# Kernel tuning notes

Measured on AMD Instinct MI355X. Metric: run time of the kernel, lower is better.

Reference implementation:

```python
import jax, jax.numpy as jnp
import numpy as np
import math

ANSWER_LEN = 11; D_MODEL = 6; FFN_DIM = 3; HEAD_DIM = 3; MAX_SEQ_LEN = 34
N_HEADS = 2; POS_DIM = 3; TOK_DIM = 3; VOCAB_SIZE = 14; MAX_DIGITS = 10
EOS_TOKEN = 12; EQUALS_TOKEN = 11; PAD_TOKEN = 13; PLUS_TOKEN = 10
B, T = 65536, 34


def _spiral(i, period):
    return (math.cos(2 * math.pi * i / period), math.sin(2 * math.pi * i / period), i / max(period - 1, 1))


def _build_pos_enc():
    N_POS = 10
    pe = np.zeros((MAX_SEQ_LEN, POS_DIM), dtype=np.float32)
    for i in range(MAX_DIGITS):
        pe[i] = _spiral(i, N_POS)
    for i in range(MAX_DIGITS):
        pe[11 + i] = _spiral(i, N_POS)
    for i in range(min(ANSWER_LEN, N_POS)):
        pe[22 + i] = _spiral(i, N_POS)
    pe[32] = [0.0, 0.0, 1.5]
    pe[10] = [2.0, 0.0, -1.0]
    pe[21] = [0.0, 2.0, -1.0]
    pe[33] = [-2.0, 0.0, -1.0]
    return pe


def _build_tok_emb():
    emb = np.zeros((VOCAB_SIZE, TOK_DIM), dtype=np.float32)
    for d in range(10):
        emb[d] = _spiral(d, 10)
    emb[PLUS_TOKEN] = [2.0, 0.0, -1.0]
    emb[EQUALS_TOKEN] = [0.0, 2.0, -1.0]
    emb[EOS_TOKEN] = [-2.0, 0.0, -1.0]
    emb[PAD_TOKEN] = [0.0, -2.0, -1.0]
    return emb


def setup_inputs() -> dict:
    key = jax.random.key(0)
    ks = jax.random.split(key, 12)
    H = N_HEADS * HEAD_DIM  # 6

    def lin(k, out_d, in_d):
        bound = 1.0 / math.sqrt(in_d)
        return jax.random.uniform(k, (out_d, in_d), jnp.float32, -bound, bound)

    return {
        'idx': jax.random.randint(ks[0], (B, T), 0, VOCAB_SIZE),
        'tok_emb': jnp.asarray(_build_tok_emb()),
        'pos_enc': jnp.asarray(_build_pos_enc()),
        'q_w': lin(ks[1], H, POS_DIM),
        'k_w': lin(ks[2], H, POS_DIM),
        'v_w': lin(ks[3], H, TOK_DIM),
        'out_w': lin(ks[4], D_MODEL, H),
        'ln1_g': jnp.ones((D_MODEL,)), 'ln1_b': jnp.zeros((D_MODEL,)),
        'ln2_g': jnp.ones((D_MODEL,)), 'ln2_b': jnp.zeros((D_MODEL,)),
        'lnf_g': jnp.ones((D_MODEL,)), 'lnf_b': jnp.zeros((D_MODEL,)),
        'ffn_w1': lin(ks[5], FFN_DIM, D_MODEL),
        'ffn_b1': jax.random.uniform(ks[6], (FFN_DIM,), jnp.float32, -1/math.sqrt(D_MODEL), 1/math.sqrt(D_MODEL)),
        'ffn_w2': lin(ks[7], D_MODEL, FFN_DIM),
        'ffn_b2': jax.random.uniform(ks[8], (D_MODEL,), jnp.float32, -1/math.sqrt(FFN_DIM), 1/math.sqrt(FFN_DIM)),
        'head_w': lin(ks[9], TOK_DIM, D_MODEL),
    }


def _ln(x, g, b, eps=1e-5):
    mu = jnp.mean(x, -1, keepdims=True)
    var = jnp.mean((x - mu) ** 2, -1, keepdims=True)
    return (x - mu) * jax.lax.rsqrt(var + eps) * g + b


def reference(idx, tok_emb, pos_enc, q_w, k_w, v_w, out_w,
              ln1_g, ln1_b, ln2_g, ln2_b, lnf_g, lnf_b,
              ffn_w1, ffn_b1, ffn_w2, ffn_b2, head_w):
    b, t = idx.shape
    tok = tok_emb[idx]                              # [B,T,3]
    pos = jnp.broadcast_to(pos_enc[:t][None], (b, t, POS_DIM))
    x = jnp.concatenate([tok, pos], -1)             # [B,T,6]
    h = _ln(x, ln1_g, ln1_b)
    x_tok, x_pos = h[..., :TOK_DIM], h[..., TOK_DIM:]
    q = (x_pos @ q_w.T).reshape(b, t, N_HEADS, HEAD_DIM)
    k = (x_pos @ k_w.T).reshape(b, t, N_HEADS, HEAD_DIM)
    v = (x_tok @ v_w.T).reshape(b, t, N_HEADS, HEAD_DIM)
    attn = jnp.einsum('bqhd,bkhd->bhqk', q, k) / math.sqrt(HEAD_DIM)
    mask = jnp.tril(jnp.ones((t, t), dtype=bool))
    attn = jnp.where(mask[None, None], attn, -jnp.inf)
    attn = jax.nn.softmax(attn, -1)
    out = jnp.einsum('bhqk,bkhd->bqhd', attn, v).reshape(b, t, N_HEADS * HEAD_DIM)
    x = x + out @ out_w.T
    h2 = _ln(x, ln2_g, ln2_b)
    ffn = jax.nn.gelu(h2 @ ffn_w1.T + ffn_b1, approximate=False) @ ffn_w2.T + ffn_b2
    x = x + ffn
    x = _ln(x, lnf_g, lnf_b)
    return (x @ head_w.T) @ tok_emb.T               # [B,T,VOCAB]
```

## Files before the change

kernel.cpp:

```cpp
#include <hip/hip_runtime.h>
#include <math.h>

#define TT  34
#define VV  14
#define BLK 256

typedef float v2f __attribute__((ext_vector_type(2)));
typedef float v4f __attribute__((ext_vector_type(4)));

#if __has_builtin(__builtin_amdgcn_exp2f)
#define EXP2F(x) __builtin_amdgcn_exp2f(x)
#else
#define EXP2F(x) exp2f(x)
#endif
#if __has_builtin(__builtin_amdgcn_rcpf)
#define RCPF(x) __builtin_amdgcn_rcpf(x)
#else
#define RCPF(x) (1.0f/(x))
#endif

static __device__ __forceinline__ v2f fma2(v2f a, v2f b, v2f c) {
    return __builtin_elementwise_fma(a, b, c);
}
static __device__ __forceinline__ v2f bc2(float s) { v2f r; r.x = s; r.y = s; return r; }
#define SV2(v, a, b) __builtin_shufflevector((v), (v), (a), (b))


__global__ __launch_bounds__(BLK) void addtx_fwd(
    const int*   __restrict__ idx,
    const float* __restrict__ tok_emb,
    const float* __restrict__ pos_enc,
    const float* __restrict__ q_w,
    const float* __restrict__ k_w,
    const float* __restrict__ v_w,
    const float* __restrict__ out_w,
    const float* __restrict__ ln1_g, const float* __restrict__ ln1_b,
    const float* __restrict__ ln2_g, const float* __restrict__ ln2_b,
    const float* __restrict__ lnf_g, const float* __restrict__ lnf_b,
    const float* __restrict__ ffn_w1, const float* __restrict__ ffn_b1,
    const float* __restrict__ ffn_w2, const float* __restrict__ ffn_b2,
    const float* __restrict__ head_w,
    float* __restrict__ out)
{
    __shared__ v4f   kvs[TT * VV * 3];
    __shared__ float wsm[308];
    __shared__ int   idsb[308];

    const int tid = threadIdx.x;
    const int blk = blockIdx.x;

    for (int i = tid; i < 308; i += BLK) {
        float val = 0.0f;
        if (i < 36)       { const int j = i / 6, d = i - j * 6; val = out_w[d * 6 + j]; }
        else if (i < 42)  val = ln2_g[i - 36];
        else if (i < 48)  val = ln2_b[i - 42];
        else if (i < 60)  { const int k = i - 48, d = k >> 1, ii = k & 1; val = ffn_w1[ii * 6 + d]; }
        else if (i < 66)  val = ffn_w1[12 + (i - 60)];
        else if (i < 69)  val = ffn_b1[i - 66];
        else if (i < 70)  val = 0.0f;
        else if (i < 88)  { const int k = i - 70, ii = k / 6, d = k - ii * 6; val = ffn_w2[d * 3 + ii]; }
        else if (i < 94)  val = ffn_b2[i - 88];
        else if (i < 96)  val = 0.0f;
        else if (i < 108) { const int k = i - 96, d = k >> 1, c = k & 1; val = lnf_g[d] * head_w[c * 6 + d]; }
        else if (i < 114) { const int d = i - 108; val = lnf_g[d] * head_w[12 + d]; }
        else if (i < 118) val = 0.0f;
        else if (i < 121) { const int c = i - 118; float s = 0.0f;
                            #pragma unroll
                            for (int d = 0; d < 6; ++d) s += lnf_b[d] * head_w[c * 6 + d];
                            val = s; }
        else if (i < 122) val = 0.0f;
        else if (i < 164) { const int k = i - 122, c = k / 14, v = k - c * 14; val = tok_emb[v * 3 + c]; }
        else if (i < 206) val = tok_emb[i - 164];
        else              val = pos_enc[i - 206];
        wsm[i] = val;
    }

    const int ntot = (int)gridDim.x * BLK;
    const int b0   = (blk * BLK) / TT;
    {
        const int gb = b0 * TT;
        for (int e = tid; e < 308; e += BLK) {
            const int g = gb + e;
            idsb[e] = (g < ntot) ? (idx[g] * 48) : 0;
        }
    }

    const float rs3l = 0.57735026918962576f * 1.4426950408889634f;
    for (int e = tid; e < TT * VV; e += BLK) {
        const int pos = e / VV, id = e - pos * VV;
        float x[6];
        x[0] = tok_emb[id * 3 + 0]; x[1] = tok_emb[id * 3 + 1]; x[2] = tok_emb[id * 3 + 2];
        x[3] = pos_enc[pos * 3 + 0]; x[4] = pos_enc[pos * 3 + 1]; x[5] = pos_enc[pos * 3 + 2];
        float mu = (x[0] + x[1] + x[2] + x[3] + x[4] + x[5]) * (1.0f / 6.0f);
        float var = 0.0f;
        #pragma unroll
        for (int d = 0; d < 6; ++d) { float dd = x[d] - mu; var += dd * dd; }
        const float rstd = rsqrtf(var * (1.0f / 6.0f) + 1e-5f);
        float h[6];
        #pragma unroll
        for (int d = 0; d < 6; ++d) h[d] = (x[d] - mu) * rstd * ln1_g[d] + ln1_b[d];
        float kk[6], vvv[6];
        #pragma unroll
        for (int r = 0; r < 6; ++r) {
            kk[r]  = (h[3] * k_w[r * 3 + 0] + h[4] * k_w[r * 3 + 1] + h[5] * k_w[r * 3 + 2]) * rs3l;
            vvv[r] =  h[0] * v_w[r * 3 + 0] + h[1] * v_w[r * 3 + 1] + h[2] * v_w[r * 3 + 2];
        }
        v4f f0; f0.x = kk[0]; f0.y = kk[3]; f0.z = kk[1]; f0.w = kk[4];
        v4f f1; f1.x = kk[2]; f1.y = kk[5]; f1.z = vvv[0]; f1.w = vvv[3];
        v4f f2; f2.x = vvv[1]; f2.y = vvv[4]; f2.z = vvv[2]; f2.w = vvv[5];
        kvs[e * 3 + 0] = f0;
        kvs[e * 3 + 1] = f1;
        kvs[e * 3 + 2] = f2;
    }
    __syncthreads();

    const int srank = (tid + ((blk & 3) << 6)) & (BLK - 1);
    const int r0 = (blk * BLK) % TT;
    const int m  = (TT - r0) % TT;
    int dsel, ksel;
    if (m < 18) {
        const int nA = (18 - m) << 3;
        if (srank < nA)            { dsel = m + (srank >> 3); ksel = srank & 7; }
        else if (srank < nA + 112) { const int r = srank - nA;       dsel = 18 + r / 7; ksel = r % 7; }
        else                       { const int r = srank - nA - 112; dsel = r >> 3;     ksel = r & 7; }
    } else {
        const int nA = (TT - m) * 7;
        if (srank < nA)            { dsel = m + srank / 7; ksel = srank % 7; }
        else if (srank < nA + 144) { const int r = srank - nA;       dsel = r >> 3;     ksel = r & 7; }
        else                       { const int r = srank - nA - 144; dsel = 18 + r / 7; ksel = r % 7; }
    }
    const int il   = dsel + ksel * TT;
    const int flat = blk * BLK + il;
    const int b    = flat / TT;
    const int t    = flat - b * TT;
    const int* __restrict__ rowL = idsb + (b - b0) * TT;

    float x[6];
    {
        const int tb = rowL[t] >> 4;
        x[0] = wsm[164 + tb]; x[1] = wsm[165 + tb]; x[2] = wsm[166 + tb];
        x[3] = wsm[206 + t * 3]; x[4] = wsm[207 + t * 3]; x[5] = wsm[208 + t * 3];
    }
    float q[6];
    {
        float mu = (x[0] + x[1] + x[2] + x[3] + x[4] + x[5]) * (1.0f / 6.0f);
        float var = 0.0f;
        #pragma unroll
        for (int d = 0; d < 6; ++d) { float dd = x[d] - mu; var += dd * dd; }
        const float rstd = rsqrtf(var * (1.0f / 6.0f) + 1e-5f);
        const float h3 = (x[3] - mu) * rstd * ln1_g[3] + ln1_b[3];
        const float h4 = (x[4] - mu) * rstd * ln1_g[4] + ln1_b[4];
        const float h5 = (x[5] - mu) * rstd * ln1_g[5] + ln1_b[5];
        #pragma unroll
        for (int r = 0; r < 6; ++r)
            q[r] = h3 * q_w[r * 3 + 0] + h4 * q_w[r * 3 + 1] + h5 * q_w[r * 3 + 2];
    }
    const v2f Q03 = {q[0], q[3]}, Q14 = {q[1], q[4]}, Q25 = {q[2], q[5]};

    v2f L = {0.f, 0.f}, A0 = {0.f, 0.f}, A1 = {0.f, 0.f}, A2 = {0.f, 0.f};
    int ids48 = rowL[0];
    const char* kp = (const char*)kvs;
    for (int s = 0; s <= t; ++s) {
        const v4f* e4 = (const v4f*)(kp + ids48);
        const v4f ka = e4[0], kb = e4[1], vb = e4[2];
        ids48 = rowL[s + 1];
        v2f sc = fma2(Q03, SV2(ka, 0, 1),
                 fma2(Q14, SV2(ka, 2, 3),
                      Q25 * SV2(kb, 0, 1)));
        v2f p; p.x = EXP2F(sc.x); p.y = EXP2F(sc.y);
        L += p;
        A0 = fma2(p, SV2(kb, 2, 3), A0);
        A1 = fma2(p, SV2(vb, 0, 1), A1);
        A2 = fma2(p, SV2(vb, 2, 3), A2);
        kp += VV * 48;
    }
    v2f I; I.x = RCPF(L.x); I.y = RCPF(L.y);
    const v2f O0 = A0 * I, O1 = A1 * I, O2 = A2 * I;
    const float o6[6] = {O0.x, O1.x, O2.x, O0.y, O1.y, O2.y};

    v2f X0 = {x[0], x[1]}, X1 = {x[2], x[3]}, X2 = {x[4], x[5]};
    #define LD2(i) (*reinterpret_cast<const v2f*>(&wsm[(i)]))
    #pragma unroll
    for (int j = 0; j < 6; ++j) {
        const v2f oj = bc2(o6[j]);
        X0 = fma2(oj, LD2(j * 6 + 0), X0);
        X1 = fma2(oj, LD2(j * 6 + 2), X1);
        X2 = fma2(oj, LD2(j * 6 + 4), X2);
    }

    {
        v2f S = X0 + X1 + X2;
        const float mu = (S.x + S.y) * (1.0f / 6.0f);
        const v2f muv = bc2(mu);
        const v2f D0 = X0 - muv, D1 = X1 - muv, D2 = X2 - muv;
        v2f E = fma2(D0, D0, fma2(D1, D1, D2 * D2));
        const float rstd = rsqrtf((E.x + E.y) * (1.0f / 6.0f) + 1e-5f);
        const v2f rs = bc2(rstd);
        const v2f H0 = fma2(D0 * rs, LD2(36), LD2(42));
        const v2f H1 = fma2(D1 * rs, LD2(38), LD2(44));
        const v2f H2 = fma2(D2 * rs, LD2(40), LD2(46));
        const float h[6] = {H0.x, H0.y, H1.x, H1.y, H2.x, H2.y};
        v2f F = LD2(66);
        float f2 = wsm[68];
        #pragma unroll
        for (int d = 0; d < 6; ++d) {
            F  = fma2(bc2(h[d]), LD2(48 + 2 * d), F);
            f2 = fmaf(h[d], wsm[60 + d], f2);
        }
        float g3[3];
        g3[0] = 0.5f * F.x * (1.0f + erff(F.x * 0.70710678118654752f));
        g3[1] = 0.5f * F.y * (1.0f + erff(F.y * 0.70710678118654752f));
        g3[2] = 0.5f * f2  * (1.0f + erff(f2  * 0.70710678118654752f));
        X0 += LD2(88); X1 += LD2(90); X2 += LD2(92);
        #pragma unroll
        for (int i = 0; i < 3; ++i) {
            const v2f gi = bc2(g3[i]);
            X0 = fma2(gi, LD2(70 + i * 6 + 0), X0);
            X1 = fma2(gi, LD2(70 + i * 6 + 2), X1);
            X2 = fma2(gi, LD2(70 + i * 6 + 4), X2);
        }
    }

    v2f lgv[7];
    {
        v2f S = X0 + X1 + X2;
        const float mu = (S.x + S.y) * (1.0f / 6.0f);
        const v2f muv = bc2(mu);
        const v2f D0 = X0 - muv, D1 = X1 - muv, D2 = X2 - muv;
        v2f E = fma2(D0, D0, fma2(D1, D1, D2 * D2));
        const float rstd = rsqrtf((E.x + E.y) * (1.0f / 6.0f) + 1e-5f);
        const float xd[6] = {D0.x, D0.y, D1.x, D1.y, D2.x, D2.y};
        v2f D01 = {0.f, 0.f};
        float d2 = 0.f;
        #pragma unroll
        for (int d = 0; d < 6; ++d) {
            D01 = fma2(bc2(xd[d]), LD2(96 + 2 * d), D01);
            d2  = fmaf(xd[d], wsm[108 + d], d2);
        }
        const v2f y01 = fma2(bc2(rstd), D01, LD2(118));
        const float y2 = fmaf(rstd, d2, wsm[120]);
        const v2f Y0 = bc2(y01.x), Y1 = bc2(y01.y), Y2 = bc2(y2);
        #pragma unroll
        for (int mm = 0; mm < 7; ++mm)
            lgv[mm] = fma2(Y0, LD2(122 + 2 * mm),
                      fma2(Y1, LD2(136 + 2 * mm),
                           Y2 * LD2(150 + 2 * mm)));
    }
    __syncthreads();

    v2f* lg2 = reinterpret_cast<v2f*>(kvs);
    #pragma unroll
    for (int j = 0; j < 7; ++j)
        lg2[il * 7 + j] = lgv[j];
    __syncthreads();
    const v2f* s2 = reinterpret_cast<const v2f*>(kvs);
    v2f* __restrict__ ob2 = reinterpret_cast<v2f*>(out + (size_t)blk * (BLK * VV));
    #pragma unroll
    for (int j = 0; j < 7; ++j)
        ob2[j * BLK + tid] = s2[j * BLK + tid];
}

extern "C" void kernel_launch(void* const* d_in, const int* in_sizes, int n_in,
                              void* d_out, int out_size, void* d_ws, size_t ws_size,
                              hipStream_t stream) {
    const int*   idx     = (const int*)  d_in[0];
    const float* tok_emb = (const float*)d_in[1];
    const float* pos_enc = (const float*)d_in[2];
    const float* q_w     = (const float*)d_in[3];
    const float* k_w     = (const float*)d_in[4];
    const float* v_w     = (const float*)d_in[5];
    const float* out_w   = (const float*)d_in[6];
    const float* ln1_g   = (const float*)d_in[7];
    const float* ln1_b   = (const float*)d_in[8];
    const float* ln2_g   = (const float*)d_in[9];
    const float* ln2_b   = (const float*)d_in[10];
    const float* lnf_g   = (const float*)d_in[11];
    const float* lnf_b   = (const float*)d_in[12];
    const float* ffn_w1  = (const float*)d_in[13];
    const float* ffn_b1  = (const float*)d_in[14];
    const float* ffn_w2  = (const float*)d_in[15];
    const float* ffn_b2  = (const float*)d_in[16];
    const float* head_w  = (const float*)d_in[17];
    float* out = (float*)d_out;

    const int n = in_sizes[0];
    const int blocks = n / BLK;
    addtx_fwd<<<blocks, BLK, 0, stream>>>(idx, tok_emb, pos_enc, q_w, k_w, v_w, out_w,
                                          ln1_g, ln1_b, ln2_g, ln2_b, lnf_g, lnf_b,
                                          ffn_w1, ffn_b1, ffn_w2, ffn_b2, head_w, out);
}
```

Baseline: 213.3 us.

## Process two adjacent query positions per thread sharing K/V loads

Each thread now handles a pair of consecutive positions (t0, t0+1) in the same sequence, sharing the K/V shared-memory reads across both queries in the attention loop. The grid is halved (512 positions per block), which amortizes per-block LDS table setup over more work. The shared-memory transpose for output staging is removed, and results are written directly to global with vector stores. This raises register pressure and makes the stores less coalesced, and the thread-to-pair assignment changes the load balance across lanes.

```diff
diff --git a/kernel.cpp b/kernel.cpp
--- a/kernel.cpp
+++ b/kernel.cpp
@@ -4,6 +4,7 @@
 #define TT  34
 #define VV  14
 #define BLK 256
+#define NPB 512
 
 typedef float v2f __attribute__((ext_vector_type(2)));
 typedef float v4f __attribute__((ext_vector_type(4)));
@@ -24,7 +25,118 @@
 }
 static __device__ __forceinline__ v2f bc2(float s) { v2f r; r.x = s; r.y = s; return r; }
 #define SV2(v, a, b) __builtin_shufflevector((v), (v), (a), (b))
-
+#define LD2(i) (*reinterpret_cast<const v2f*>(&wsm[(i)]))
+
+
+static __device__ __forceinline__ void epi_store(
+    const float* __restrict__ wsm, const float o6[6], const float x[6],
+    float* __restrict__ outp, int elem1)
+{
+    v2f X0 = {x[0], x[1]}, X1 = {x[2], x[3]}, X2 = {x[4], x[5]};
+    #pragma unroll
+    for (int j = 0; j < 6; ++j) {
+        const v2f oj = bc2(o6[j]);
+        X0 = fma2(oj, LD2(j * 6 + 0), X0);
+        X1 = fma2(oj, LD2(j * 6 + 2), X1);
+        X2 = fma2(oj, LD2(j * 6 + 4), X2);
+    }
+    {
+        v2f S = X0 + X1 + X2;
+        const float mu = (S.x + S.y) * (1.0f / 6.0f);
+        const v2f muv = bc2(mu);
+        const v2f D0 = X0 - muv, D1 = X1 - muv, D2 = X2 - muv;
+        v2f E = fma2(D0, D0, fma2(D1, D1, D2 * D2));
+        const float rstd = rsqrtf((E.x + E.y) * (1.0f / 6.0f) + 1e-5f);
+        const v2f rs = bc2(rstd);
+        const v2f H0 = fma2(D0 * rs, LD2(36), LD2(42));
+        const v2f H1 = fma2(D1 * rs, LD2(38), LD2(44));
+        const v2f H2 = fma2(D2 * rs, LD2(40), LD2(46));
+        const float h[6] = {H0.x, H0.y, H1.x, H1.y, H2.x, H2.y};
+        v2f F = LD2(66);
+        float f2 = wsm[68];
+        #pragma unroll
+        for (int d = 0; d < 6; ++d) {
+            F  = fma2(bc2(h[d]), LD2(48 + 2 * d), F);
+            f2 = fmaf(h[d], wsm[60 + d], f2);
+        }
+        float g3[3];
+        g3[0] = 0.5f * F.x * (1.0f + erff(F.x * 0.70710678118654752f));
+        g3[1] = 0.5f * F.y * (1.0f + erff(F.y * 0.70710678118654752f));
+        g3[2] = 0.5f * f2  * (1.0f + erff(f2  * 0.70710678118654752f));
+        X0 += LD2(88); X1 += LD2(90); X2 += LD2(92);
+        #pragma unroll
+        for (int i = 0; i < 3; ++i) {
+            const v2f gi = bc2(g3[i]);
+            X0 = fma2(gi, LD2(70 + i * 6 + 0), X0);
+            X1 = fma2(gi, LD2(70 + i * 6 + 2), X1);
+            X2 = fma2(gi, LD2(70 + i * 6 + 4), X2);
+        }
+    }
+    v2f lgv[7];
+    {
+        v2f S = X0 + X1 + X2;
+        const float mu = (S.x + S.y) * (1.0f / 6.0f);
+        const v2f muv = bc2(mu);
+        const v2f D0 = X0 - muv, D1 = X1 - muv, D2 = X2 - muv;
+        v2f E = fma2(D0, D0, fma2(D1, D1, D2 * D2));
+        const float rstd = rsqrtf((E.x + E.y) * (1.0f / 6.0f) + 1e-5f);
+        const float xd[6] = {D0.x, D0.y, D1.x, D1.y, D2.x, D2.y};
+        v2f D01 = {0.f, 0.f};
+        float d2 = 0.f;
+        #pragma unroll
+        for (int d = 0; d < 6; ++d) {
+            D01 = fma2(bc2(xd[d]), LD2(96 + 2 * d), D01);
+            d2  = fmaf(xd[d], wsm[108 + d], d2);
+        }
+        const v2f y01 = fma2(bc2(rstd), D01, LD2(118));
+        const float y2 = fmaf(rstd, d2, wsm[120]);
+        const v2f Y0 = bc2(y01.x), Y1 = bc2(y01.y), Y2 = bc2(y2);
+        #pragma unroll
+        for (int mm = 0; mm < 7; ++mm)
+            lgv[mm] = fma2(Y0, LD2(122 + 2 * mm),
+                      fma2(Y1, LD2(136 + 2 * mm),
+                           Y2 * LD2(150 + 2 * mm)));
+    }
+    if (!elem1) {
+        v4f w0; w0.x = lgv[0].x; w0.y = lgv[0].y; w0.z = lgv[1].x; w0.w = lgv[1].y;
+        v4f w1; w1.x = lgv[2].x; w1.y = lgv[2].y; w1.z = lgv[3].x; w1.w = lgv[3].y;
+        v4f w2; w2.x = lgv[4].x; w2.y = lgv[4].y; w2.z = lgv[5].x; w2.w = lgv[5].y;
+        *reinterpret_cast<v4f*>(outp + 0) = w0;
+        *reinterpret_cast<v4f*>(outp + 4) = w1;
+        *reinterpret_cast<v4f*>(outp + 8) = w2;
+        *reinterpret_cast<v2f*>(outp + 12) = lgv[6];
+    } else {
+        *reinterpret_cast<v2f*>(outp + 0) = lgv[0];
+        v4f w0; w0.x = lgv[1].x; w0.y = lgv[1].y; w0.z = lgv[2].x; w0.w = lgv[2].y;
+        v4f w1; w1.x = lgv[3].x; w1.y = lgv[3].y; w1.z = lgv[4].x; w1.w = lgv[4].y;
+        v4f w2; w2.x = lgv[5].x; w2.y = lgv[5].y; w2.z = lgv[6].x; w2.w = lgv[6].y;
+        *reinterpret_cast<v4f*>(outp + 2)  = w0;
+        *reinterpret_cast<v4f*>(outp + 6)  = w1;
+        *reinterpret_cast<v4f*>(outp + 10) = w2;
+    }
+}
+
+static __device__ __forceinline__ void make_q(
+    const float* __restrict__ ln1_g, const float* __restrict__ ln1_b,
+    const float* __restrict__ q_w, const float x[6],
+    v2f& Q03, v2f& Q14, v2f& Q25)
+{
+    float mu = (x[0] + x[1] + x[2] + x[3] + x[4] + x[5]) * (1.0f / 6.0f);
+    float var = 0.0f;
+    #pragma unroll
+    for (int d = 0; d < 6; ++d) { float dd = x[d] - mu; var += dd * dd; }
+    const float rstd = rsqrtf(var * (1.0f / 6.0f) + 1e-5f);
+    const float h3 = (x[3] - mu) * rstd * ln1_g[3] + ln1_b[3];
+    const float h4 = (x[4] - mu) * rstd * ln1_g[4] + ln1_b[4];
+    const float h5 = (x[5] - mu) * rstd * ln1_g[5] + ln1_b[5];
+    float q[6];
+    #pragma unroll
+    for (int r = 0; r < 6; ++r)
+        q[r] = h3 * q_w[r * 3 + 0] + h4 * q_w[r * 3 + 1] + h5 * q_w[r * 3 + 2];
+    Q03.x = q[0]; Q03.y = q[3];
+    Q14.x = q[1]; Q14.y = q[4];
+    Q25.x = q[2]; Q25.y = q[5];
+}
 
 __global__ __launch_bounds__(BLK) void addtx_fwd(
     const int*   __restrict__ idx,
@@ -40,11 +152,11 @@
     const float* __restrict__ ffn_w1, const float* __restrict__ ffn_b1,
     const float* __restrict__ ffn_w2, const float* __restrict__ ffn_b2,
     const float* __restrict__ head_w,
-    float* __restrict__ out)
+    float* __restrict__ out, int n)
 {
     __shared__ v4f   kvs[TT * VV * 3];
     __shared__ float wsm[308];
-    __shared__ int   idsb[308];
+    __shared__ int   idsb[17 * TT];
 
     const int tid = threadIdx.x;
     const int blk = blockIdx.x;
@@ -75,13 +187,13 @@
         wsm[i] = val;
     }
 
-    const int ntot = (int)gridDim.x * BLK;
-    const int b0   = (blk * BLK) / TT;
+    const int p0 = blk * BLK;
+    const int b0 = p0 / 17;
     {
         const int gb = b0 * TT;
-        for (int e = tid; e < 308; e += BLK) {
+        for (int e = tid; e < 17 * TT; e += BLK) {
             const int g = gb + e;
-            idsb[e] = (g < ntot) ? (idx[g] * 48) : 0;
+            idsb[e] = (g < n) ? (idx[g] * 48) : 0;
         }
     }
 
@@ -115,149 +227,76 @@
     __syncthreads();
 
     const int srank = (tid + ((blk & 3) << 6)) & (BLK - 1);
-    const int r0 = (blk * BLK) % TT;
-    const int m  = (TT - r0) % TT;
-    int dsel, ksel;
-    if (m < 18) {
-        const int nA = (18 - m) << 3;
-        if (srank < nA)            { dsel = m + (srank >> 3); ksel = srank & 7; }
-        else if (srank < nA + 112) { const int r = srank - nA;       dsel = 18 + r / 7; ksel = r % 7; }
-        else                       { const int r = srank - nA - 112; dsel = r >> 3;     ksel = r & 7; }
-    } else {
-        const int nA = (TT - m) * 7;
-        if (srank < nA)            { dsel = m + srank / 7; ksel = srank % 7; }
-        else if (srank < nA + 144) { const int r = srank - nA;       dsel = r >> 3;     ksel = r & 7; }
-        else                       { const int r = srank - nA - 144; dsel = 18 + r / 7; ksel = r % 7; }
-    }
-    const int il   = dsel + ksel * TT;
-    const int flat = blk * BLK + il;
-    const int b    = flat / TT;
-    const int t    = flat - b * TT;
+    const int r0 = p0 % 17;
+    const int thrA = 15 * r0;
+    int u, k;
+    if (srank < thrA)           { u = srank / 15;      k = srank - 15 * u; }
+    else if (srank < thrA + 16) { u = r0;              k = srank - thrA;   }
+    else                        { const int rr = srank - 1; u = rr / 15; k = rr - 15 * u; }
+    int dd17 = u - r0; if (dd17 < 0) dd17 += 17;
+    const int pl = dd17 + 17 * k;
+    const int p  = p0 + pl;
+    const int b  = p / 17;
+    const int t0 = 2 * (p - b * 17);
+    const int t1 = t0 + 1;
     const int* __restrict__ rowL = idsb + (b - b0) * TT;
 
-    float x[6];
-    {
-        const int tb = rowL[t] >> 4;
-        x[0] = wsm[164 + tb]; x[1] = wsm[165 + tb]; x[2] = wsm[166 + tb];
-        x[3] = wsm[206 + t * 3]; x[4] = wsm[207 + t * 3]; x[5] = wsm[208 + t * 3];
-    }
-    float q[6];
-    {
-        float mu = (x[0] + x[1] + x[2] + x[3] + x[4] + x[5]) * (1.0f / 6.0f);
-        float var = 0.0f;
-        #pragma unroll
-        for (int d = 0; d < 6; ++d) { float dd = x[d] - mu; var += dd * dd; }
-        const float rstd = rsqrtf(var * (1.0f / 6.0f) + 1e-5f);
-        const float h3 = (x[3] - mu) * rstd * ln1_g[3] + ln1_b[3];
-        const float h4 = (x[4] - mu) * rstd * ln1_g[4] + ln1_b[4];
-        const float h5 = (x[5] - mu) * rstd * ln1_g[5] + ln1_b[5];
-        #pragma unroll
-        for (int r = 0; r < 6; ++r)
-            q[r] = h3 * q_w[r * 3 + 0] + h4 * q_w[r * 3 + 1] + h5 * q_w[r * 3 + 2];
-    }
-    const v2f Q03 = {q[0], q[3]}, Q14 = {q[1], q[4]}, Q25 = {q[2], q[5]};
-
-    v2f L = {0.f, 0.f}, A0 = {0.f, 0.f}, A1 = {0.f, 0.f}, A2 = {0.f, 0.f};
+    float xa[6], xb[6];
+    {
+        const int ta3 = rowL[t0] >> 4;
+        const int tb3 = rowL[t1] >> 4;
+        xa[0] = wsm[164 + ta3]; xa[1] = wsm[165 + ta3]; xa[2] = wsm[166 + ta3];
+        xb[0] = wsm[164 + tb3]; xb[1] = wsm[165 + tb3]; xb[2] = wsm[166 + tb3];
+        xa[3] = wsm[206 + t0 * 3]; xa[4] = wsm[207 + t0 * 3]; xa[5] = wsm[208 + t0 * 3];
+        xb[3] = wsm[206 + t1 * 3]; xb[4] = wsm[207 + t1 * 3]; xb[5] = wsm[208 + t1 * 3];
+    }
+    v2f Q03a, Q14a, Q25a, Q03b, Q14b, Q25b;
+    make_q(ln1_g, ln1_b, q_w, xa, Q03a, Q14a, Q25a);
+    make_q(ln1_g, ln1_b, q_w, xb, Q03b, Q14b, Q25b);
+
+    v2f La = {0.f, 0.f}, A0a = {0.f, 0.f}, A1a = {0.f, 0.f}, A2a = {0.f, 0.f};
+    v2f Lb = {0.f, 0.f}, A0b = {0.f, 0.f}, A1b = {0.f, 0.f}, A2b = {0.f, 0.f};
     int ids48 = rowL[0];
     const char* kp = (const char*)kvs;
-    for (int s = 0; s <= t; ++s) {
+    for (int s = 0; s <= t0; ++s) {
         const v4f* e4 = (const v4f*)(kp + ids48);
         const v4f ka = e4[0], kb = e4[1], vb = e4[2];
         ids48 = rowL[s + 1];
-        v2f sc = fma2(Q03, SV2(ka, 0, 1),
-                 fma2(Q14, SV2(ka, 2, 3),
-                      Q25 * SV2(kb, 0, 1)));
-        v2f p; p.x = EXP2F(sc.x); p.y = EXP2F(sc.y);
-        L += p;
-        A0 = fma2(p, SV2(kb, 2, 3), A0);
-        A1 = fma2(p, SV2(vb, 0, 1), A1);
-        A2 = fma2(p, SV2(vb, 2, 3), A2);
+        const v2f ka01 = SV2(ka, 0, 1), ka23 = SV2(ka, 2, 3);
+        const v2f kb01 = SV2(kb, 0, 1), kb23 = SV2(kb, 2, 3);
+        const v2f vb01 = SV2(vb, 0, 1), vb23 = SV2(vb, 2, 3);
+        v2f sa = fma2(Q03a, ka01, fma2(Q14a, ka23, Q25a * kb01));
+        v2f sb = fma2(Q03b, ka01, fma2(Q14b, ka23, Q25b * kb01));
+        v2f pa; pa.x = EXP2F(sa.x); pa.y = EXP2F(sa.y);
+        v2f pb; pb.x = EXP2F(sb.x); pb.y = EXP2F(sb.y);
+        La += pa; Lb += pb;
+        A0a = fma2(pa, kb23, A0a); A0b = fma2(pb, kb23, A0b);
+        A1a = fma2(pa, vb01, A1a); A1b = fma2(pb, vb01, A1b);
+        A2a = fma2(pa, vb23, A2a); A2b = fma2(pb, vb23, A2b);
         kp += VV * 48;
     }
-    v2f I; I.x = RCPF(L.x); I.y = RCPF(L.y);
-    const v2f O0 = A0 * I, O1 = A1 * I, O2 = A2 * I;
-    const float o6[6] = {O0.x, O1.x, O2.x, O0.y, O1.y, O2.y};
-
-    v2f X0 = {x[0], x[1]}, X1 = {x[2], x[3]}, X2 = {x[4], x[5]};
-    #define LD2(i) (*reinterpret_cast<const v2f*>(&wsm[(i)]))
-    #pragma unroll
-    for (int j = 0; j < 6; ++j) {
-        const v2f oj = bc2(o6[j]);
-        X0 = fma2(oj, LD2(j * 6 + 0), X0);
-        X1 = fma2(oj, LD2(j * 6 + 2), X1);
-        X2 = fma2(oj, LD2(j * 6 + 4), X2);
-    }
-
-    {
-        v2f S = X0 + X1 + X2;
-        const float mu = (S.x + S.y) * (1.0f / 6.0f);
-        const v2f muv = bc2(mu);
-        const v2f D0 = X0 - muv, D1 = X1 - muv, D2 = X2 - muv;
-        v2f E = fma2(D0, D0, fma2(D1, D1, D2 * D2));
-        const float rstd = rsqrtf((E.x + E.y) * (1.0f / 6.0f) + 1e-5f);
-        const v2f rs = bc2(rstd);
-        const v2f H0 = fma2(D0 * rs, LD2(36), LD2(42));
-        const v2f H1 = fma2(D1 * rs, LD2(38), LD2(44));
-        const v2f H2 = fma2(D2 * rs, LD2(40), LD2(46));
-        const float h[6] = {H0.x, H0.y, H1.x, H1.y, H2.x, H2.y};
-        v2f F = LD2(66);
-        float f2 = wsm[68];
-        #pragma unroll
-        for (int d = 0; d < 6; ++d) {
-            F  = fma2(bc2(h[d]), LD2(48 + 2 * d), F);
-            f2 = fmaf(h[d], wsm[60 + d], f2);
-        }
-        float g3[3];
-        g3[0] = 0.5f * F.x * (1.0f + erff(F.x * 0.70710678118654752f));
-        g3[1] = 0.5f * F.y * (1.0f + erff(F.y * 0.70710678118654752f));
-        g3[2] = 0.5f * f2  * (1.0f + erff(f2  * 0.70710678118654752f));
-        X0 += LD2(88); X1 += LD2(90); X2 += LD2(92);
-        #pragma unroll
-        for (int i = 0; i < 3; ++i) {
-            const v2f gi = bc2(g3[i]);
-            X0 = fma2(gi, LD2(70 + i * 6 + 0), X0);
-            X1 = fma2(gi, LD2(70 + i * 6 + 2), X1);
-            X2 = fma2(gi, LD2(70 + i * 6 + 4), X2);
-        }
-    }
-
-    v2f lgv[7];
-    {
-        v2f S = X0 + X1 + X2;
-        const float mu = (S.x + S.y) * (1.0f / 6.0f);
-        const v2f muv = bc2(mu);
-        const v2f D0 = X0 - muv, D1 = X1 - muv, D2 = X2 - muv;
-        v2f E = fma2(D0, D0, fma2(D1, D1, D2 * D2));
-        const float rstd = rsqrtf((E.x + E.y) * (1.0f / 6.0f) + 1e-5f);
-        const float xd[6] = {D0.x, D0.y, D1.x, D1.y, D2.x, D2.y};
-        v2f D01 = {0.f, 0.f};
-        float d2 = 0.f;
-        #pragma unroll
-        for (int d = 0; d < 6; ++d) {
-            D01 = fma2(bc2(xd[d]), LD2(96 + 2 * d), D01);
-            d2  = fmaf(xd[d], wsm[108 + d], d2);
-        }
-        const v2f y01 = fma2(bc2(rstd), D01, LD2(118));
-        const float y2 = fmaf(rstd, d2, wsm[120]);
-        const v2f Y0 = bc2(y01.x), Y1 = bc2(y01.y), Y2 = bc2(y2);
-        #pragma unroll
-        for (int mm = 0; mm < 7; ++mm)
-            lgv[mm] = fma2(Y0, LD2(122 + 2 * mm),
-                      fma2(Y1, LD2(136 + 2 * mm),
-                           Y2 * LD2(150 + 2 * mm)));
-    }
-    __syncthreads();
-
-    v2f* lg2 = reinterpret_cast<v2f*>(kvs);
-    #pragma unroll
-    for (int j = 0; j < 7; ++j)
-        lg2[il * 7 + j] = lgv[j];
-    __syncthreads();
-    const v2f* s2 = reinterpret_cast<const v2f*>(kvs);
-    v2f* __restrict__ ob2 = reinterpret_cast<v2f*>(out + (size_t)blk * (BLK * VV));
-    #pragma unroll
-    for (int j = 0; j < 7; ++j)
-        ob2[j * BLK + tid] = s2[j * BLK + tid];
+    {
+        const v4f* e4 = (const v4f*)(kp + ids48);
+        const v4f ka = e4[0], kb = e4[1], vb = e4[2];
+        v2f sb = fma2(Q03b, SV2(ka, 0, 1),
+                 fma2(Q14b, SV2(ka, 2, 3), Q25b * SV2(kb, 0, 1)));
+        v2f pb; pb.x = EXP2F(sb.x); pb.y = EXP2F(sb.y);
+        Lb += pb;
+        A0b = fma2(pb, SV2(kb, 2, 3), A0b);
+        A1b = fma2(pb, SV2(vb, 0, 1), A1b);
+        A2b = fma2(pb, SV2(vb, 2, 3), A2b);
+    }
+
+    v2f Ia; Ia.x = RCPF(La.x); Ia.y = RCPF(La.y);
+    v2f Ib; Ib.x = RCPF(Lb.x); Ib.y = RCPF(Lb.y);
+    const v2f Oa0 = A0a * Ia, Oa1 = A1a * Ia, Oa2 = A2a * Ia;
+    const v2f Ob0 = A0b * Ib, Ob1 = A1b * Ib, Ob2 = A2b * Ib;
+    const float o6a[6] = {Oa0.x, Oa1.x, Oa2.x, Oa0.y, Oa1.y, Oa2.y};
+    const float o6b[6] = {Ob0.x, Ob1.x, Ob2.x, Ob0.y, Ob1.y, Ob2.y};
+
+    float* __restrict__ outp = out + (size_t)(b * TT + t0) * VV;
+    epi_store(wsm, o6a, xa, outp,      0);
+    epi_store(wsm, o6b, xb, outp + VV, 1);
 }
 
 extern "C" void kernel_launch(void* const* d_in, const int* in_sizes, int n_in,
@@ -284,8 +323,8 @@
     float* out = (float*)d_out;
 
     const int n = in_sizes[0];
-    const int blocks = n / BLK;
+    const int blocks = n / NPB;
     addtx_fwd<<<blocks, BLK, 0, stream>>>(idx, tok_emb, pos_enc, q_w, k_w, v_w, out_w,
                                           ln1_g, ln1_b, ln2_g, ln2_b, lnf_g, lnf_b,
-                                          ffn_w1, ffn_b1, ffn_w2, ffn_b2, head_w, out);
-}
+                                          ffn_w1, ffn_b1, ffn_w2, ffn_b2, head_w, out, n);
+}
```

After: 218.6 us. 2.5% more time.

## Double block size to 512 and rework thread-to-position mapping for larger tiles

Applied to the files above, without the earlier changes.

Raises the block size from 256 to 512 threads and adds an occupancy hint to launch_bounds. The per-block K/V table precompute and weight staging are amortised over twice as many output positions, which roughly halves the redundant setup work per element. The thread-to-(batch, position) assignment is rewritten for the new block size, and the total element count is passed in explicitly. The larger tile needs bigger shared buffers, and the new mapping logic risks different store coalescing or bank conflicts.

```diff
diff --git a/kernel.cpp b/kernel.cpp
--- a/kernel.cpp
+++ b/kernel.cpp
@@ -3,7 +3,7 @@
 
 #define TT  34
 #define VV  14
-#define BLK 256
+#define BLK 512
 
 typedef float v2f __attribute__((ext_vector_type(2)));
 typedef float v4f __attribute__((ext_vector_type(4)));
@@ -26,7 +26,7 @@
 #define SV2(v, a, b) __builtin_shufflevector((v), (v), (a), (b))
 
 
-__global__ __launch_bounds__(BLK) void addtx_fwd(
+__global__ __launch_bounds__(BLK, 8) void addtx_fwd(
     const int*   __restrict__ idx,
     const float* __restrict__ tok_emb,
     const float* __restrict__ pos_enc,
@@ -40,16 +40,17 @@
     const float* __restrict__ ffn_w1, const float* __restrict__ ffn_b1,
     const float* __restrict__ ffn_w2, const float* __restrict__ ffn_b2,
     const float* __restrict__ head_w,
-    float* __restrict__ out)
+    float* __restrict__ out, int n)
 {
-    __shared__ v4f   kvs[TT * VV * 3];
+    __shared__ v4f   kvs[1792];
     __shared__ float wsm[308];
-    __shared__ int   idsb[308];
+    __shared__ int   idsb[594];
 
     const int tid = threadIdx.x;
     const int blk = blockIdx.x;
 
-    for (int i = tid; i < 308; i += BLK) {
+    if (tid < 308) {
+        const int i = tid;
         float val = 0.0f;
         if (i < 36)       { const int j = i / 6, d = i - j * 6; val = out_w[d * 6 + j]; }
         else if (i < 42)  val = ln2_g[i - 36];
@@ -75,13 +76,13 @@
         wsm[i] = val;
     }
 
-    const int ntot = (int)gridDim.x * BLK;
-    const int b0   = (blk * BLK) / TT;
+    const int p0 = blk * BLK;
+    const int b0 = p0 / TT;
     {
         const int gb = b0 * TT;
-        for (int e = tid; e < 308; e += BLK) {
+        for (int e = tid; e < 594; e += BLK) {
             const int g = gb + e;
-            idsb[e] = (g < ntot) ? (idx[g] * 48) : 0;
+            idsb[e] = (g < n) ? (idx[g] * 48) : 0;
         }
     }
 
@@ -114,25 +115,17 @@
     }
     __syncthreads();
 
-    const int srank = (tid + ((blk & 3) << 6)) & (BLK - 1);
-    const int r0 = (blk * BLK) % TT;
-    const int m  = (TT - r0) % TT;
-    int dsel, ksel;
-    if (m < 18) {
-        const int nA = (18 - m) << 3;
-        if (srank < nA)            { dsel = m + (srank >> 3); ksel = srank & 7; }
-        else if (srank < nA + 112) { const int r = srank - nA;       dsel = 18 + r / 7; ksel = r % 7; }
-        else                       { const int r = srank - nA - 112; dsel = r >> 3;     ksel = r & 7; }
-    } else {
-        const int nA = (TT - m) * 7;
-        if (srank < nA)            { dsel = m + srank / 7; ksel = srank % 7; }
-        else if (srank < nA + 144) { const int r = srank - nA;       dsel = r >> 3;     ksel = r & 7; }
-        else                       { const int r = srank - nA - 144; dsel = 18 + r / 7; ksel = r % 7; }
-    }
-    const int il   = dsel + ksel * TT;
-    const int flat = blk * BLK + il;
+    const int srank = (tid + ((blk & 7) << 6)) & (BLK - 1);
+    const int r0 = p0 % TT;
+    const int thrA = 15 * r0;
+    int t, dlt, ksel;
+    if (srank < thrA)           { t = srank / 15; ksel = srank - 15 * t; dlt = t - r0 + TT; }
+    else if (srank < thrA + 32) { const int rr = srank - thrA; dlt = rr >> 4; ksel = rr & 15; t = r0 + dlt; }
+    else                        { const int rr = srank - thrA - 32; const int qq = rr / 15;
+                                  ksel = rr - 15 * qq; dlt = 2 + qq; t = r0 + dlt; }
+    const int il   = dlt + TT * ksel;
+    const int flat = p0 + il;
     const int b    = flat / TT;
-    const int t    = flat - b * TT;
     const int* __restrict__ rowL = idsb + (b - b0) * TT;
 
     float x[6];
@@ -287,5 +280,5 @@
     const int blocks = n / BLK;
     addtx_fwd<<<blocks, BLK, 0, stream>>>(idx, tok_emb, pos_enc, q_w, k_w, v_w, out_w,
                                           ln1_g, ln1_b, ln2_g, ln2_b, lnf_g, lnf_b,
-                                          ffn_w1, ffn_b1, ffn_w2, ffn_b2, head_w, out);
+                                          ffn_w1, ffn_b1, ffn_w2, ffn_b2, head_w, out, n);
 }
```

Result: no change. 212.2 us (-0.5%).
